# Kernel tuning notes

Measured on AMD Instinct MI355X. Metric: run time of the kernel, lower is better.

Reference implementation:

```python
import jax, jax.numpy as jnp
import numpy as np

N = 1 << 20   # number of values to quantize
K = 256       # codebook size (8-bit)


def setup_inputs() -> dict:
    key = jax.random.key(0)
    kx, kc = jax.random.split(key)
    x = jax.random.normal(kx, (N,), dtype=jnp.float32)
    centers = jax.random.normal(kc, (K,), dtype=jnp.float32)
    return {"x": x, "centers": centers}


def reference(x, centers):
    # (x[:, None] - centers[None, :]).abs().argmin(dim=1)
    # -> index of nearest scalar codebook entry per element, shape (N,)
    diff = jnp.abs(x[:, None] - centers[None, :])  # (N, K)
    return jnp.argmin(diff, axis=1)
```

## Files before the change

kernel.cpp:

```cpp
#include <hip/hip_runtime.h>

#define N_ELEM (1 << 20)
#define K 256
#define BLOCK 256
#define EPT 4
#define GRID (N_ELEM / (BLOCK * EPT))


__global__ __launch_bounds__(K) void sort_centers_kernel(
    const float*  __restrict__ centers,
    float*        __restrict__ ws_val,
    float2*       __restrict__ ws_pair)
{
    __shared__ float sc[K];
    const int t = threadIdx.x;
    const float c = centers[t];
    sc[t] = c;
    __syncthreads();

    int rank = 0;
#pragma unroll 16
    for (int j = 0; j < K; ++j) {
        float cj = sc[j];
        rank += (cj < c) || (cj == c && j < t);
    }
    ws_val[rank]  = c;
    ws_pair[rank] = make_float2(c, __int_as_float(t));
}

__global__ __launch_bounds__(BLOCK) void argmin_bsearch_kernel(
    const float*  __restrict__ x,
    const float*  __restrict__ ws_val,
    const float2* __restrict__ ws_pair,
    int*          __restrict__ out)
{
    __shared__ float s_val[K];
    __shared__ alignas(8) float2 s_pair[K];
    const int t = threadIdx.x;
    s_val[t]  = ws_val[t];
    s_pair[t] = ws_pair[t];
    __syncthreads();

    const float v127 = ws_val[127];
    const float v63  = ws_val[63],  v191 = ws_val[191];
    const float v31  = ws_val[31],  v95  = ws_val[95];
    const float v159 = ws_val[159], v223 = ws_val[223];

    const int base = (blockIdx.x * BLOCK + t) * EPT;
    float4 v = *reinterpret_cast<const float4*>(x + base);
    float xs[EPT] = {v.x, v.y, v.z, v.w};
    int res[EPT];

#pragma unroll
    for (int e = 0; e < EPT; ++e) {
        const float xv = xs[e];

        int pos = (v127 < xv) ? 128 : 0;
        const float la = (pos & 128) ? v191 : v63;
        pos += (la < xv) ? 64 : 0;
        const float lb = (pos & 64) ? ((pos & 128) ? v223 : v95)
                                    : ((pos & 128) ? v159 : v31);
        pos += (lb < xv) ? 32 : 0;

#pragma unroll
        for (int s = 16; s > 0; s >>= 1)
            pos += (s_val[pos + s - 1] < xv) ? s : 0;
        pos += (s_val[pos] < xv) ? 1 : 0;

        const int il = (pos > 0) ? pos - 1 : 0;
        const int ir = (pos < K) ? pos     : K - 1;
        const float2 pl = s_pair[il];
        const float2 pr = s_pair[ir];
        const float dl = fabsf(xv - pl.x);
        const float dr = fabsf(xv - pr.x);
        const int ol  = __float_as_int(pl.y);
        const int orr = __float_as_int(pr.y);
        res[e] = (dl < dr) ? ol : ((dr < dl) ? orr : min(ol, orr));
    }

    *reinterpret_cast<int4*>(out + base) = make_int4(res[0], res[1], res[2], res[3]);
}

extern "C" void kernel_launch(void* const* d_in, const int* in_sizes, int n_in,
                              void* d_out, int out_size, void* d_ws, size_t ws_size,
                              hipStream_t stream)
{
    const float* x       = (const float*)d_in[0];
    const float* centers = (const float*)d_in[1];
    int*         out     = (int*)d_out;

    float*  ws_val  = (float*)d_ws;
    float2* ws_pair = (float2*)(ws_val + K);

    sort_centers_kernel<<<1, K, 0, stream>>>(centers, ws_val, ws_pair);
    argmin_bsearch_kernel<<<GRID, BLOCK, 0, stream>>>(x, ws_val, ws_pair, out);
}
```

Measured before the change: 67.87 us.

## Fuse codebook sort into the search kernel and raise elements per thread

Drops the separate single-block sort kernel and has every block rank-sort the 256 centers itself, reading them from global memory before doing its binary searches. Elements per thread go from 4 to 16, which cuts the grid to 256 blocks so the redundant per-block sort is spread over more work. The x loads are issued before the sort so their latency overlaps it. This removes one kernel launch and the serial dependency on the sort. The cost is repeated 256-step sort work in every block and lower parallelism from the smaller grid.

```diff
diff --git a/kernel.cpp b/kernel.cpp
--- a/kernel.cpp
+++ b/kernel.cpp
@@ -3,52 +3,42 @@
 #define N_ELEM (1 << 20)
 #define K 256
 #define BLOCK 256
-#define EPT 4
+#define EPT 16
 #define GRID (N_ELEM / (BLOCK * EPT))
 
-
-__global__ __launch_bounds__(K) void sort_centers_kernel(
-    const float*  __restrict__ centers,
-    float*        __restrict__ ws_val,
-    float2*       __restrict__ ws_pair)
-{
-    __shared__ float sc[K];
-    const int t = threadIdx.x;
-    const float c = centers[t];
-    sc[t] = c;
-    __syncthreads();
-
-    int rank = 0;
-#pragma unroll 16
-    for (int j = 0; j < K; ++j) {
-        float cj = sc[j];
-        rank += (cj < c) || (cj == c && j < t);
-    }
-    ws_val[rank]  = c;
-    ws_pair[rank] = make_float2(c, __int_as_float(t));
-}
-
-__global__ __launch_bounds__(BLOCK) void argmin_bsearch_kernel(
-    const float*  __restrict__ x,
-    const float*  __restrict__ ws_val,
-    const float2* __restrict__ ws_pair,
-    int*          __restrict__ out)
+__global__ __launch_bounds__(BLOCK) void kmeans_fused_kernel(
+    const float* __restrict__ x,
+    const float* __restrict__ centers,
+    int*         __restrict__ out)
 {
     __shared__ float s_val[K];
     __shared__ alignas(8) float2 s_pair[K];
     const int t = threadIdx.x;
-    s_val[t]  = ws_val[t];
-    s_pair[t] = ws_pair[t];
+    const int base = (blockIdx.x * BLOCK + t) * EPT;
+
+    float4 v0 = *reinterpret_cast<const float4*>(x + base);
+    float4 v1 = *reinterpret_cast<const float4*>(x + base + 4);
+    float4 v2 = *reinterpret_cast<const float4*>(x + base + 8);
+    float4 v3 = *reinterpret_cast<const float4*>(x + base + 12);
+
+    const float c = centers[t];
+    int rank = 0;
+#pragma unroll 16
+    for (int j = 0; j < K; ++j) {
+        const float cj = centers[j];
+        rank += ((cj < c) || (cj == c && j < t)) ? 1 : 0;
+    }
+    s_val[rank]  = c;
+    s_pair[rank] = make_float2(c, __int_as_float(t));
     __syncthreads();
 
-    const float v127 = ws_val[127];
-    const float v63  = ws_val[63],  v191 = ws_val[191];
-    const float v31  = ws_val[31],  v95  = ws_val[95];
-    const float v159 = ws_val[159], v223 = ws_val[223];
+    const float v127 = s_val[127];
+    const float v63  = s_val[63],  v191 = s_val[191];
+    const float v31  = s_val[31],  v95  = s_val[95];
+    const float v159 = s_val[159], v223 = s_val[223];
 
-    const int base = (blockIdx.x * BLOCK + t) * EPT;
-    float4 v = *reinterpret_cast<const float4*>(x + base);
-    float xs[EPT] = {v.x, v.y, v.z, v.w};
+    float xs[EPT] = {v0.x, v0.y, v0.z, v0.w, v1.x, v1.y, v1.z, v1.w,
+                     v2.x, v2.y, v2.z, v2.w, v3.x, v3.y, v3.z, v3.w};
     int res[EPT];
 
 #pragma unroll
@@ -78,7 +68,10 @@
         res[e] = (dl < dr) ? ol : ((dr < dl) ? orr : min(ol, orr));
     }
 
-    *reinterpret_cast<int4*>(out + base) = make_int4(res[0], res[1], res[2], res[3]);
+    *reinterpret_cast<int4*>(out + base)      = make_int4(res[0],  res[1],  res[2],  res[3]);
+    *reinterpret_cast<int4*>(out + base + 4)  = make_int4(res[4],  res[5],  res[6],  res[7]);
+    *reinterpret_cast<int4*>(out + base + 8)  = make_int4(res[8],  res[9],  res[10], res[11]);
+    *reinterpret_cast<int4*>(out + base + 12) = make_int4(res[12], res[13], res[14], res[15]);
 }
 
 extern "C" void kernel_launch(void* const* d_in, const int* in_sizes, int n_in,
@@ -89,9 +82,5 @@
     const float* centers = (const float*)d_in[1];
     int*         out     = (int*)d_out;
 
-    float*  ws_val  = (float*)d_ws;
-    float2* ws_pair = (float2*)(ws_val + K);
-
-    sort_centers_kernel<<<1, K, 0, stream>>>(centers, ws_val, ws_pair);
-    argmin_bsearch_kernel<<<GRID, BLOCK, 0, stream>>>(x, ws_val, ws_pair, out);
+    kmeans_fused_kernel<<<GRID, BLOCK, 0, stream>>>(x, centers, out);
 }
```

Measured after the change: 69.01 us. No clear change (+1.7%).
